# Performance work log

Hardware: AMD Instinct MI355X
Metric: run time of the kernel (lower is better)

The kernel has to match this reference:

```python
import jax, jax.numpy as jnp
import numpy as np

K = 20
SLOPE = 0.2  # LeakyReLU negative slope used by DGCNN edge convs


def _knn_idx(x, k):
    # x: [C, N]. Returns [N, k] indices of nearest neighbors by L2 distance
    # (includes self), matching torch topk of -pairwise_dist.
    xx = jnp.sum(x * x, axis=0)                      # [N]
    neg_dist = 2.0 * (x.T @ x) - xx[:, None] - xx[None, :]  # [N, N]
    return jax.lax.top_k(neg_dist, k)[1]


def _graph_feature(x, k):
    # x: [C, N] -> edge features [2C, N, k] = concat(x_j - x_i, x_i)
    idx = _knn_idx(x, k)                             # [N, k]
    nb = x[:, idx]                                   # [C, N, k] gather
    xc = jnp.broadcast_to(x[:, :, None], nb.shape)   # [C, N, k]
    return jnp.concatenate([nb - xc, xc], axis=0)


def _edge_conv(x, w, s, c, k):
    # 1x1 Conv2d (no bias) + eval-mode BN folded into per-channel (s, c)
    # + LeakyReLU, then max over the k neighbors.
    f = _graph_feature(x, k)                         # [2C, N, k]
    y = jnp.einsum('oc,cnk->onk', w, f)              # [Co, N, k]
    y = jax.nn.leaky_relu(y * s[:, None, None] + c[:, None, None], SLOPE)
    return jnp.max(y, axis=-1)                       # [Co, N]


def setup_inputs() -> dict:
    key = jax.random.key(0)
    ks = jax.random.split(key, 25)
    N = 16384
    f32 = jnp.float32

    def w(k, shape):
        return jax.random.normal(k, shape, dtype=f32) * 0.05

    def scale(k, shape):
        return 1.0 + 0.1 * jax.random.uniform(k, shape, dtype=f32)

    return {
        'coords': jax.random.normal(ks[0], (N, 3), dtype=f32),
        'feats': jax.random.uniform(ks[1], (N, 1), dtype=f32),
        'w1': w(ks[2], (64, 8)),    's1': scale(ks[3], (64,)),  'c1': w(ks[4], (64,)),
        'w2': w(ks[5], (64, 128)),  's2': scale(ks[6], (64,)),  'c2': w(ks[7], (64,)),
        'w3': w(ks[8], (128, 128)), 's3': scale(ks[9], (128,)), 'c3': w(ks[10], (128,)),
        'w4': w(ks[11], (256, 256)),'s4': scale(ks[12], (256,)),'c4': w(ks[13], (256,)),
        'w5': w(ks[14], (512, 512)),'s5': scale(ks[15], (512,)),'c5': w(ks[16], (512,)),
        'wf': w(ks[17], (3, 256, 512)), 'sf': scale(ks[18], (3, 256)), 'cf': w(ks[19], (3, 256)),
        'wsem': w(ks[20], (20, 256)), 'bsem': w(ks[21], (20,)),
    }


def reference(coords, feats, w1, s1, c1, w2, s2, c2, w3, s3, c3,
              w4, s4, c4, w5, s5, c5, wf, sf, cf, wsem, bsem):
    # Single-cloud batch (batch_size=1): x_input = cat(coords, feats).T -> [4, N]
    x0 = jnp.concatenate([coords.T, feats.T], axis=0)        # [4, N]
    x1 = _edge_conv(x0, w1, s1, c1, K)                       # [64, N]
    x2 = _edge_conv(x1, w2, s2, c2, K)                       # [64, N]
    x3 = _edge_conv(x2, w3, s3, c3, K)                       # [128, N]
    x4 = _edge_conv(x3, w4, s4, c4, K)                       # [256, N]
    cat = jnp.concatenate([x1, x2, x3, x4], axis=0)          # [512, N]
    x5 = jax.nn.leaky_relu(
        jnp.einsum('oc,cn->on', w5, cat) * s5[:, None] + c5[:, None], SLOPE)

    # Multi-scale feat_layers + out_bn (eval-mode BN folded to sf, cf)
    ms_feats = (jnp.einsum('soc,cn->son', wf, x5)
                * sf[:, :, None] + cf[:, :, None])           # [3, 256, N]

    # sem_head on the last scale's features
    sem_feat = ms_feats[-1].T                                # [N, 256]
    sem_logits = (sem_feat @ wsem.T + bsem)[None]            # [1, N, 20]

    ms_coords = jnp.broadcast_to(coords[None], (3,) + coords.shape)  # [3, N, 3]
    ms_masks = jnp.zeros((3, coords.shape[0]), dtype=bool)           # [3, N]
    return ms_feats, ms_coords, ms_masks, sem_logits
```

## Files before the change

kernel.cpp:

```cpp
#include <hip/hip_runtime.h>
#include <hip/hip_bf16.h>
#include <cmath>

#define K_NN 20
#define SLOPE 0.2f
#define NSEG 8
#define TK 16
#define SCAP 8

typedef _Float16 h8 __attribute__((ext_vector_type(8)));
typedef _Float16 h4 __attribute__((ext_vector_type(4)));
typedef float f4v __attribute__((ext_vector_type(4)));

__device__ __forceinline__ float lrelu(float x) { return x > 0.f ? x : SLOPE * x; }

__device__ __forceinline__ void topk_insert(float (&bd)[K_NN], int (&bi)[K_NN], float nd, int ji) {
  bool c[K_NN];
#pragma unroll
  for (int j = 0; j < K_NN; ++j) c[j] = nd > bd[j];
#pragma unroll
  for (int j = K_NN - 1; j >= 1; --j) {
    bd[j] = c[j] ? (c[j - 1] ? bd[j - 1] : nd) : bd[j];
    bi[j] = c[j] ? (c[j - 1] ? bi[j - 1] : ji) : bi[j];
  }
  bd[0] = c[0] ? nd : bd[0];
  bi[0] = c[0] ? ji : bi[0];
}

__global__ void build_x0_coords(const float* __restrict__ coords, const float* __restrict__ feats,
                                float* __restrict__ x0, float* __restrict__ oC,
                                float* __restrict__ oM, int N) {
  int n = blockIdx.x * 256 + threadIdx.x;
  if (n >= N) return;
  float c0 = coords[n * 3 + 0], c1 = coords[n * 3 + 1], c2 = coords[n * 3 + 2];
  float f = feats[n];
  float4 v = make_float4(c0, c1, c2, f);
  *(float4*)(x0 + (size_t)n * 4) = v;
#pragma unroll
  for (int s = 0; s < 3; ++s) {
    size_t b = (size_t)s * N * 3 + (size_t)n * 3;
    oC[b + 0] = c0; oC[b + 1] = c1; oC[b + 2] = c2;
    oM[(size_t)s * N + n] = 0.f;
  }
}

__global__ void compute_xx(const float* __restrict__ x, int ld, int C,
                           float* __restrict__ xx, int N) {
  int n = blockIdx.x * 256 + threadIdx.x;
  if (n >= N) return;
  const float* r = x + (size_t)n * ld;
  float s = 0.f;
  for (int c = 0; c < C; c += 4) {
    float4 v = *(const float4*)(r + c);
    s += v.x * v.x; s += v.y * v.y; s += v.z * v.z; s += v.w * v.w;
  }
  xx[n] = s;
}

template <int C>
__global__ void prep_hl(const float* __restrict__ x, int ld, _Float16* __restrict__ xh,
                        _Float16* __restrict__ xl, int N) {
  constexpr int C4 = C / 4;
  int i = blockIdx.x * 256 + threadIdx.x;
  if (i >= N * C4) return;
  int n = i / C4, c4 = i % C4;
  float4 v = *(const float4*)(x + (size_t)n * ld + c4 * 4);
  h4 hh, ll;
  hh[0] = (_Float16)v.x; ll[0] = (_Float16)(v.x - (float)hh[0]);
  hh[1] = (_Float16)v.y; ll[1] = (_Float16)(v.y - (float)hh[1]);
  hh[2] = (_Float16)v.z; ll[2] = (_Float16)(v.z - (float)hh[2]);
  hh[3] = (_Float16)v.w; ll[3] = (_Float16)(v.w - (float)hh[3]);
  *(h4*)(xh + (size_t)n * C + c4 * 4) = hh;
  *(h4*)(xl + (size_t)n * C + c4 * 4) = ll;
}

template <int C>
__global__ __launch_bounds__(256, 2) void knn_seg(
    const float* __restrict__ xP, int ld, const float* __restrict__ xx,
    float* __restrict__ pd, int* __restrict__ pi, int N, int segLen) {
  constexpr int T = 64;
  __shared__ float tile[T * C];
  __shared__ float txx[T];
  __shared__ float sd_st[SCAP * 256];
  __shared__ int si_st[SCAP * 256];
  int tid = threadIdx.x;
  int q = blockIdx.x * 256 + tid;
  int j0 = blockIdx.y * segLen;

  float4 qv[C / 4];
#pragma unroll
  for (int c4 = 0; c4 < C / 4; ++c4) qv[c4] = *(const float4*)(xP + (size_t)q * ld + c4 * 4);
  float xxq = xx[q];

  float bd[K_NN]; int bi[K_NN];
#pragma unroll
  for (int k = 0; k < K_NN; ++k) { bd[k] = -INFINITY; bi[k] = 0; }
  float thr = -INFINITY;
  int cnt = 0;

  for (int jt = j0; jt < j0 + segLen; jt += T) {
    constexpr int TOT4 = T * C / 4;
    for (int f = tid; f < TOT4; f += 256) {
      int t = f / (C / 4), c4 = f % (C / 4);
      *(float4*)(tile + t * C + c4 * 4) = *(const float4*)(xP + (size_t)(jt + t) * ld + c4 * 4);
    }
    if (tid < T) txx[tid] = xx[jt + tid];
    __syncthreads();
#pragma unroll 2
    for (int t = 0; t < T; ++t) {
      const float4* rp = (const float4*)(tile + t * C);
      float dot = 0.f;
#pragma unroll
      for (int c4 = 0; c4 < C / 4; ++c4) {
        float4 v = rp[c4];
        dot += qv[c4].x * v.x; dot += qv[c4].y * v.y;
        dot += qv[c4].z * v.z; dot += qv[c4].w * v.w;
      }
      float nd = 2.f * dot - xxq - txx[t];
      if (nd > thr) {
        sd_st[cnt * 256 + tid] = nd;
        si_st[cnt * 256 + tid] = jt + t;
        cnt++;
      }
      if (__any(cnt == SCAP)) {
        for (int e = 0; e < cnt; ++e) {
          float dnd = sd_st[e * 256 + tid];
          int dji = si_st[e * 256 + tid];
          if (dnd > bd[K_NN - 1]) topk_insert(bd, bi, dnd, dji);
        }
        cnt = 0;
        thr = bd[K_NN - 1];
      }
    }
    __syncthreads();
  }
  for (int e = 0; e < cnt; ++e) {
    float dnd = sd_st[e * 256 + tid];
    int dji = si_st[e * 256 + tid];
    if (dnd > bd[K_NN - 1]) topk_insert(bd, bi, dnd, dji);
  }

  size_t base = ((size_t)blockIdx.y * N + q) * K_NN;
#pragma unroll
  for (int k = 0; k < K_NN; ++k) { pd[base + k] = bd[k]; pi[base + k] = bi[k]; }
}

__global__ void knn_merge(const float* __restrict__ pd, const int* __restrict__ pi,
                          int* __restrict__ idx, int N, int S) {
  int q = blockIdx.x * 256 + threadIdx.x;
  if (q >= N) return;
  float bd[K_NN]; int bi[K_NN];
#pragma unroll
  for (int k = 0; k < K_NN; ++k) { bd[k] = -INFINITY; bi[k] = 0; }
  for (int s = 0; s < S; ++s) {
    size_t base = ((size_t)s * N + q) * K_NN;
    for (int k = 0; k < K_NN; ++k) {
      float nd = pd[base + k];
      if (!(nd > bd[K_NN - 1])) break;
      topk_insert(bd, bi, nd, pi[base + k]);
    }
  }
#pragma unroll
  for (int k = 0; k < K_NN; ++k) idx[(size_t)q * K_NN + k] = bi[k];
}

template <int C>
__global__ __launch_bounds__(512, 2) void knn_mfma(
    const _Float16* __restrict__ xh, const _Float16* __restrict__ xl,
    const float* __restrict__ xx, int* __restrict__ idx, int N) {
  constexpr int SLOTS = C / 8;
  constexpr int SWM = SLOTS - 1;
  constexpr int NCH = C / 32;
  constexpr int TILE_UNITS = 2 * 32 * SLOTS;
  constexpr int UPT = TILE_UNITS / 256;
  constexpr int STAGE_B = 2 * 2 * TILE_UNITS * 16;
  constexpr int MERGE_B = 64 * 8 * K_NN * 8;
  constexpr int LDS_B = (STAGE_B + 32768 > MERGE_B) ? STAGE_B + 32768 : MERGE_B;
  __shared__ char lds[LDS_B];
  float* sd_st = (float*)(lds + STAGE_B);
  int* si_st = (int*)(lds + STAGE_B + 16384);

  int tid = threadIdx.x;
  int wv = tid >> 6, lane = tid & 63;
  int qh = wv >> 1, ch = wv & 1;
  int lj = lane & 15, g = lane >> 4;
  int q0 = blockIdx.x * 64;
  int q = q0 + qh * 16 + lj;
  int chbase = ch * (N / 2);
  const int NT = (N / 2) / 32;

  h8 bh[NCH], bl[NCH];
#pragma unroll
  for (int m = 0; m < NCH; ++m) {
    bh[m] = *(const h8*)(xh + (size_t)q * C + m * 32 + g * 8);
    bl[m] = *(const h8*)(xl + (size_t)q * C + m * 32 + g * 8);
  }
  float qxx = xx[q];

  float bd[K_NN]; int bi[K_NN];
#pragma unroll
  for (int k = 0; k < K_NN; ++k) { bd[k] = -INFINITY; bi[k] = 0; }
  float thr = -INFINITY;
  int cnt = 0;

  int cidx = qh * 64 + lane;
  float4 ldr[UPT];

  auto ldreg = [&](int t) {
    int jt = chbase + t * 32;
#pragma unroll
    for (int u = 0; u < UPT; ++u) {
      int p = cidx * UPT + u;
      int part = p / (32 * SLOTS);
      int row = (p / SLOTS) & 31;
      int slot = p & SWM;
      const _Float16* src = part ? xl : xh;
      ldr[u] = *(const float4*)(src + (size_t)(jt + row) * C + (slot ^ (row & SWM)) * 8);
    }
  };
  auto dswrite = [&](int buf) {
#pragma unroll
    for (int u = 0; u < UPT; ++u) {
      int p = cidx * UPT + u;
      *(float4*)(lds + ((size_t)(ch * 2 + buf) * TILE_UNITS + p) * 16) = ldr[u];
    }
  };
  auto compute = [&](int buf, int jt) {
    float cxx[8];
#pragma unroll
    for (int s = 0; s < 2; ++s)
#pragma unroll
      for (int r = 0; r < 4; ++r) cxx[s * 4 + r] = xx[jt + s * 16 + g * 4 + r];
    char* tb = lds + (size_t)(ch * 2 + buf) * TILE_UNITS * 16;
#pragma unroll
    for (int sub = 0; sub < 2; ++sub) {
      int row = sub * 16 + lj;
      h8 ah[NCH], al[NCH];
#pragma unroll
      for (int m = 0; m < NCH; ++m) {
        int su = (m * 4 + g) ^ (row & SWM);
        ah[m] = *(const h8*)(tb + ((size_t)(0 * 32 + row) * SLOTS + su) * 16);
        al[m] = *(const h8*)(tb + ((size_t)(1 * 32 + row) * SLOTS + su) * 16);
      }
      f4v acc = {0.f, 0.f, 0.f, 0.f};
#pragma unroll
      for (int m = 0; m < NCH; ++m)
        acc = __builtin_amdgcn_mfma_f32_16x16x32_f16(ah[m], bh[m], acc, 0, 0, 0);
#pragma unroll
      for (int m = 0; m < NCH; ++m)
        acc = __builtin_amdgcn_mfma_f32_16x16x32_f16(ah[m], bl[m], acc, 0, 0, 0);
#pragma unroll
      for (int m = 0; m < NCH; ++m)
        acc = __builtin_amdgcn_mfma_f32_16x16x32_f16(al[m], bh[m], acc, 0, 0, 0);
#pragma unroll
      for (int r = 0; r < 4; ++r) {
        float d = 2.f * acc[r] - qxx - cxx[sub * 4 + r];
        if (d > thr) {
          sd_st[cnt * 512 + tid] = d;
          si_st[cnt * 512 + tid] = jt + sub * 16 + g * 4 + r;
          cnt++;
        }
        if (__any(cnt == SCAP)) {
          for (int e = 0; e < cnt; ++e) {
            float dnd = sd_st[e * 512 + tid];
            int dji = si_st[e * 512 + tid];
            if (dnd > bd[K_NN - 1]) topk_insert(bd, bi, dnd, dji);
          }
          cnt = 0;
          thr = bd[K_NN - 1];
        }
      }
    }
  };

  ldreg(0);
  dswrite(0);
  __syncthreads();
  for (int t = 0; t < NT; ++t) {
    int cur = t & 1;
    if (t + 1 < NT) ldreg(t + 1);
    compute(cur, chbase + t * 32);
    __syncthreads();
    if (t + 1 < NT) {
      dswrite(cur ^ 1);
      __syncthreads();
    }
  }
  for (int e = 0; e < cnt; ++e) {
    float dnd = sd_st[e * 512 + tid];
    int dji = si_st[e * 512 + tid];
    if (dnd > bd[K_NN - 1]) topk_insert(bd, bi, dnd, dji);
  }
  __syncthreads();

  float* mg = (float*)lds;
  int list = ch * 4 + g;
  int qlocal = qh * 16 + lj;
#pragma unroll
  for (int k = 0; k < K_NN; ++k) {
    int e = ((qlocal * 8 + list) * K_NN + k) * 2;
    mg[e] = bd[k];
    ((int*)mg)[e + 1] = bi[k];
  }
  __syncthreads();
  if (tid < 64) {
    int pr[8] = {0, 0, 0, 0, 0, 0, 0, 0};
    float hd[8]; int hx[8];
#pragma unroll
    for (int j = 0; j < 8; ++j) {
      int e = ((tid * 8 + j) * K_NN) * 2;
      hd[j] = mg[e]; hx[j] = ((int*)mg)[e + 1];
    }
    for (int k = 0; k < K_NN; ++k) {
      float best = hd[0]; int bidx = hx[0]; int bj = 0;
#pragma unroll
      for (int j = 1; j < 8; ++j) {
        bool btr = (hd[j] > best) || (hd[j] == best && hx[j] < bidx);
        best = btr ? hd[j] : best;
        bidx = btr ? hx[j] : bidx;
        bj = btr ? j : bj;
      }
      idx[(size_t)(q0 + tid) * K_NN + k] = bidx;
#pragma unroll
      for (int j = 0; j < 8; ++j) {
        if (j == bj) {
          pr[j]++;
          if (pr[j] < K_NN) {
            int e = ((tid * 8 + j) * K_NN + pr[j]) * 2;
            hd[j] = mg[e]; hx[j] = ((int*)mg)[e + 1];
          } else {
            hd[j] = -INFINITY; hx[j] = 0x7fffffff;
          }
        }
      }
    }
  }
}

__global__ void prep_wcat(const float* __restrict__ w, float* __restrict__ wcat, int O, int C) {
  int i = blockIdx.x * 256 + threadIdx.x;
  if (i >= O * C) return;
  int o = i / C, c = i % C;
  float wa = w[(size_t)o * 2 * C + c];
  float wb = w[(size_t)o * 2 * C + C + c];
  wcat[(size_t)o * C + c] = wa;
  wcat[((size_t)O + o) * C + c] = wb - wa;
}

template <int MODE>
__global__ __launch_bounds__(256) void gemm_nt(
    const float* __restrict__ A, int lda, const float* __restrict__ B, int ldb,
    float* __restrict__ Out, int ldo, int M, int Nout, int Kdim,
    const float* __restrict__ sv, const float* __restrict__ cv) {
  __shared__ float As[TK][64];
  __shared__ float Bs[TK][64];
  int tid = threadIdx.x;
  int tx = tid & 15, ty = tid >> 4;
  int m0 = blockIdx.x * 64, n0 = blockIdx.y * 64;
  int lrow = tid >> 2, lkq = tid & 3;
  float acc[4][4] = {};

  for (int k0 = 0; k0 < Kdim; k0 += TK) {
    float4 av = make_float4(0.f, 0.f, 0.f, 0.f), bv = make_float4(0.f, 0.f, 0.f, 0.f);
    if (k0 + lkq * 4 < Kdim) {
      av = *(const float4*)(A + (size_t)(m0 + lrow) * lda + k0 + lkq * 4);
      bv = *(const float4*)(B + (size_t)(n0 + lrow) * ldb + k0 + lkq * 4);
    }
    As[lkq * 4 + 0][lrow] = av.x; As[lkq * 4 + 1][lrow] = av.y;
    As[lkq * 4 + 2][lrow] = av.z; As[lkq * 4 + 3][lrow] = av.w;
    Bs[lkq * 4 + 0][lrow] = bv.x; Bs[lkq * 4 + 1][lrow] = bv.y;
    Bs[lkq * 4 + 2][lrow] = bv.z; Bs[lkq * 4 + 3][lrow] = bv.w;
    __syncthreads();
#pragma unroll
    for (int kk = 0; kk < TK; ++kk) {
      float a[4], b[4];
      *(float4*)a = *(const float4*)&As[kk][ty * 4];
      *(float4*)b = *(const float4*)&Bs[kk][tx * 4];
#pragma unroll
      for (int i = 0; i < 4; ++i)
#pragma unroll
        for (int j = 0; j < 4; ++j) acc[i][j] += a[i] * b[j];
    }
    __syncthreads();
  }

  float4 s4 = make_float4(1.f, 1.f, 1.f, 1.f), c4 = make_float4(0.f, 0.f, 0.f, 0.f);
  if (MODE != 0) {
    s4 = *(const float4*)(sv + n0 + tx * 4);
    c4 = *(const float4*)(cv + n0 + tx * 4);
  }
#pragma unroll
  for (int i = 0; i < 4; ++i) {
    float4 r = make_float4(acc[i][0], acc[i][1], acc[i][2], acc[i][3]);
    if (MODE != 0) {
      r.x = r.x * s4.x + c4.x; r.y = r.y * s4.y + c4.y;
      r.z = r.z * s4.z + c4.z; r.w = r.w * s4.w + c4.w;
    }
    if (MODE == 1) { r.x = lrelu(r.x); r.y = lrelu(r.y); r.z = lrelu(r.z); r.w = lrelu(r.w); }
    *(float4*)(Out + (size_t)(m0 + ty * 4 + i) * ldo + n0 + tx * 4) = r;
  }
}

template <int O>
__global__ void edge_max(const float* __restrict__ U, const int* __restrict__ idx,
                         const float* __restrict__ sv, const float* __restrict__ cv,
                         float* __restrict__ out, int N) {
  constexpr int TPP = O / 4;
  constexpr int PPB = 256 / TPP;
  int tid = threadIdx.x;
  int n = blockIdx.x * PPB + tid / TPP;
  int o4 = tid % TPP;
  const int* ir = idx + (size_t)n * K_NN;
  float4 m = make_float4(-INFINITY, -INFINITY, -INFINITY, -INFINITY);
#pragma unroll
  for (int k = 0; k < K_NN; ++k) {
    int j = ir[k];
    float4 t = *(const float4*)(U + (size_t)j * (2 * O) + o4 * 4);
    m.x = fmaxf(m.x, t.x); m.y = fmaxf(m.y, t.y);
    m.z = fmaxf(m.z, t.z); m.w = fmaxf(m.w, t.w);
  }
  float4 v = *(const float4*)(U + (size_t)n * (2 * O) + O + o4 * 4);
  float4 s4 = *(const float4*)(sv + o4 * 4);
  float4 c4 = *(const float4*)(cv + o4 * 4);
  float4 r;
  r.x = lrelu(s4.x * (v.x + m.x) + c4.x);
  r.y = lrelu(s4.y * (v.y + m.y) + c4.y);
  r.z = lrelu(s4.z * (v.z + m.z) + c4.z);
  r.w = lrelu(s4.w * (v.w + m.w) + c4.w);
  *(float4*)(out + (size_t)n * 512 + o4 * 4) = r;
}

__global__ void transpose_nt(const float* __restrict__ in, float* __restrict__ out, int N, int Cc) {
  __shared__ float t[32][33];
  int bx = blockIdx.x, by = blockIdx.y;
  int lx = threadIdx.x, ly = threadIdx.y;
#pragma unroll
  for (int i = 0; i < 4; ++i)
    t[ly + i * 8][lx] = in[(size_t)(by * 32 + ly + i * 8) * Cc + bx * 32 + lx];
  __syncthreads();
#pragma unroll
  for (int i = 0; i < 4; ++i)
    out[(size_t)(bx * 32 + ly + i * 8) * N + by * 32 + lx] = t[lx][ly + i * 8];
}

__global__ void sem_kernel(const float* __restrict__ T1, const float* __restrict__ wsem,
                           const float* __restrict__ bsem, float* __restrict__ out, int N) {
  int tid = threadIdx.x;
  int n = blockIdx.x * 8 + (tid >> 5);
  int g = tid & 31;
  if (g < 20) {
    const float* row = T1 + (size_t)n * 768 + 512;
    const float* wr = wsem + (size_t)g * 256;
    float acc = 0.f;
    for (int o = 0; o < 256; ++o) acc += row[o] * wr[o];
    out[(size_t)n * 20 + g] = acc + bsem[g];
  }
}

template <int C, int O>
static void run_layer_seg(const float* x, int ld, const float* wc, const float* sv,
                          const float* cv, float* outcol, float* xxb, int* idxb, float* pd,
                          int* pi, float* U, int N, hipStream_t stream) {
  compute_xx<<<N / 256, 256, 0, stream>>>(x, ld, C, xxb, N);
  knn_seg<C><<<dim3(N / 256, NSEG), 256, 0, stream>>>(x, ld, xxb, pd, pi, N, N / NSEG);
  knn_merge<<<N / 256, 256, 0, stream>>>(pd, pi, idxb, N, NSEG);
  gemm_nt<0><<<dim3(N / 64, (2 * O) / 64), 256, 0, stream>>>(x, ld, wc, C, U, 2 * O, N, 2 * O, C,
                                                             nullptr, nullptr);
  edge_max<O><<<N / (256 / (O / 4)), 256, 0, stream>>>(U, idxb, sv, cv, outcol, N);
}

template <int C, int O>
static void run_layer_mfma(const float* x, int ld, const float* wc, const float* sv,
                           const float* cv, float* outcol, float* xxb, int* idxb,
                           _Float16* xh, _Float16* xl, float* U, int N, hipStream_t stream) {
  compute_xx<<<N / 256, 256, 0, stream>>>(x, ld, C, xxb, N);
  prep_hl<C><<<(N * (C / 4)) / 256, 256, 0, stream>>>(x, ld, xh, xl, N);
  knn_mfma<C><<<N / 64, 512, 0, stream>>>(xh, xl, xxb, idxb, N);
  gemm_nt<0><<<dim3(N / 64, (2 * O) / 64), 256, 0, stream>>>(x, ld, wc, C, U, 2 * O, N, 2 * O, C,
                                                             nullptr, nullptr);
  edge_max<O><<<N / (256 / (O / 4)), 256, 0, stream>>>(U, idxb, sv, cv, outcol, N);
}

extern "C" void kernel_launch(void* const* d_in, const int* in_sizes, int n_in,
                              void* d_out, int out_size, void* d_ws, size_t ws_size,
                              hipStream_t stream) {
  const int N = in_sizes[0] / 3;
  const float* coords = (const float*)d_in[0];
  const float* feats  = (const float*)d_in[1];
  const float* w1 = (const float*)d_in[2];
  const float* s1 = (const float*)d_in[3];
  const float* c1 = (const float*)d_in[4];
  const float* w2 = (const float*)d_in[5];
  const float* s2 = (const float*)d_in[6];
  const float* c2 = (const float*)d_in[7];
  const float* w3 = (const float*)d_in[8];
  const float* s3 = (const float*)d_in[9];
  const float* c3 = (const float*)d_in[10];
  const float* w4 = (const float*)d_in[11];
  const float* s4 = (const float*)d_in[12];
  const float* c4 = (const float*)d_in[13];
  const float* w5 = (const float*)d_in[14];
  const float* s5 = (const float*)d_in[15];
  const float* c5 = (const float*)d_in[16];
  const float* wf = (const float*)d_in[17];
  const float* sf = (const float*)d_in[18];
  const float* cf = (const float*)d_in[19];
  const float* wsem = (const float*)d_in[20];
  const float* bsem = (const float*)d_in[21];

  float* base = (float*)d_ws;
  size_t off = 0;
  float* XC  = base + off; off += (size_t)N * 512;
  float* UX5 = base + off; off += (size_t)N * 512;
  float* x0  = base + off; off += (size_t)N * 4;
  float* xxb = base + off; off += (size_t)N;
  int*   idxb = (int*)(base + off); off += (size_t)N * K_NN;
  float* wc1 = base + off; off += 128 * 4;
  float* wc2 = base + off; off += 128 * 64;
  float* wc3 = base + off; off += 256 * 64;
  float* wc4 = base + off; off += 512 * 128;
  float* T1  = base + off; off += (size_t)N * 768;
  float* pd = T1;
  int*   pi = (int*)(T1 + (size_t)NSEG * N * K_NN);
  _Float16* xh = (_Float16*)UX5;
  _Float16* xl = (_Float16*)(UX5 + (size_t)N * 64);

  float* oF = (float*)d_out;
  float* oC = oF + (size_t)3 * 256 * N;
  float* oM = oC + (size_t)3 * N * 3;
  float* oL = oM + (size_t)3 * N;

  build_x0_coords<<<N / 256, 256, 0, stream>>>(coords, feats, x0, oC, oM, N);

  prep_wcat<<<(64 * 4 + 255) / 256, 256, 0, stream>>>(w1, wc1, 64, 4);
  prep_wcat<<<(64 * 64 + 255) / 256, 256, 0, stream>>>(w2, wc2, 64, 64);
  prep_wcat<<<(128 * 64 + 255) / 256, 256, 0, stream>>>(w3, wc3, 128, 64);
  prep_wcat<<<(256 * 128 + 255) / 256, 256, 0, stream>>>(w4, wc4, 256, 128);

  run_layer_seg<4, 64>(x0, 4, wc1, s1, c1, XC + 0, xxb, idxb, pd, pi, UX5, N, stream);
  run_layer_mfma<64, 64>(XC + 0, 512, wc2, s2, c2, XC + 64, xxb, idxb, xh, xl, UX5, N, stream);
  run_layer_mfma<64, 128>(XC + 64, 512, wc3, s3, c3, XC + 128, xxb, idxb, xh, xl, UX5, N, stream);
  run_layer_mfma<128, 256>(XC + 128, 512, wc4, s4, c4, XC + 256, xxb, idxb, xh, xl, UX5, N, stream);

  gemm_nt<1><<<dim3(N / 64, 8), 256, 0, stream>>>(XC, 512, w5, 512, UX5, 512, N, 512, 512, s5, c5);
  gemm_nt<2><<<dim3(N / 64, 12), 256, 0, stream>>>(UX5, 512, wf, 512, T1, 768, N, 768, 512, sf, cf);
  transpose_nt<<<dim3(24, N / 32), dim3(32, 8), 0, stream>>>(T1, oF, N, 768);
  sem_kernel<<<N / 8, 256, 0, stream>>>(T1, wsem, bsem, oL, N);
}
```

Baseline: 4.065 ms.

## Shrink knn_mfma LDS footprint and move partial-list merge to separate kernel

The in-kernel 8-way merge of partial top-k lists, which needed a large LDS region, is removed. Each wave now writes its sorted partial list to global scratch, and the existing knn_merge kernel combines them afterward. The candidate staging buffer is cut from 8 to 4 entries per thread, which flushes more often, and the tile load mapping changes to a coalesced u*256+cidx pattern. Together these lower LDS use so more blocks can be resident, at the cost of extra global traffic and another kernel launch.

Result: slower. 4.262 ms (+4.8%).

```diff
diff --git a/kernel.cpp b/kernel.cpp
--- a/kernel.cpp
+++ b/kernel.cpp
@@ -7,6 +7,7 @@
 #define NSEG 8
 #define TK 16
 #define SCAP 8
+#define SCAP_M 4
 
 typedef _Float16 h8 __attribute__((ext_vector_type(8)));
 typedef _Float16 h4 __attribute__((ext_vector_type(4)));
@@ -167,18 +168,16 @@
 template <int C>
 __global__ __launch_bounds__(512, 2) void knn_mfma(
     const _Float16* __restrict__ xh, const _Float16* __restrict__ xl,
-    const float* __restrict__ xx, int* __restrict__ idx, int N) {
+    const float* __restrict__ xx, float* __restrict__ pd, int* __restrict__ pi, int N) {
   constexpr int SLOTS = C / 8;
   constexpr int SWM = SLOTS - 1;
   constexpr int NCH = C / 32;
   constexpr int TILE_UNITS = 2 * 32 * SLOTS;
   constexpr int UPT = TILE_UNITS / 256;
   constexpr int STAGE_B = 2 * 2 * TILE_UNITS * 16;
-  constexpr int MERGE_B = 64 * 8 * K_NN * 8;
-  constexpr int LDS_B = (STAGE_B + 32768 > MERGE_B) ? STAGE_B + 32768 : MERGE_B;
-  __shared__ char lds[LDS_B];
-  float* sd_st = (float*)(lds + STAGE_B);
-  int* si_st = (int*)(lds + STAGE_B + 16384);
+  __shared__ char lds[STAGE_B];
+  __shared__ float sd_st[SCAP_M * 512];
+  __shared__ int si_st[SCAP_M * 512];
 
   int tid = threadIdx.x;
   int wv = tid >> 6, lane = tid & 63;
@@ -210,7 +209,7 @@
     int jt = chbase + t * 32;
 #pragma unroll
     for (int u = 0; u < UPT; ++u) {
-      int p = cidx * UPT + u;
+      int p = u * 256 + cidx;
       int part = p / (32 * SLOTS);
       int row = (p / SLOTS) & 31;
       int slot = p & SWM;
@@ -221,7 +220,7 @@
   auto dswrite = [&](int buf) {
 #pragma unroll
     for (int u = 0; u < UPT; ++u) {
-      int p = cidx * UPT + u;
+      int p = u * 256 + cidx;
       *(float4*)(lds + ((size_t)(ch * 2 + buf) * TILE_UNITS + p) * 16) = ldr[u];
     }
   };
@@ -260,7 +259,7 @@
           si_st[cnt * 512 + tid] = jt + sub * 16 + g * 4 + r;
           cnt++;
         }
-        if (__any(cnt == SCAP)) {
+        if (__any(cnt == SCAP_M)) {
           for (int e = 0; e < cnt; ++e) {
             float dnd = sd_st[e * 512 + tid];
             int dji = si_st[e * 512 + tid];
@@ -291,50 +290,11 @@
     int dji = si_st[e * 512 + tid];
     if (dnd > bd[K_NN - 1]) topk_insert(bd, bi, dnd, dji);
   }
-  __syncthreads();
-
-  float* mg = (float*)lds;
+
   int list = ch * 4 + g;
-  int qlocal = qh * 16 + lj;
-#pragma unroll
-  for (int k = 0; k < K_NN; ++k) {
-    int e = ((qlocal * 8 + list) * K_NN + k) * 2;
-    mg[e] = bd[k];
-    ((int*)mg)[e + 1] = bi[k];
-  }
-  __syncthreads();
-  if (tid < 64) {
-    int pr[8] = {0, 0, 0, 0, 0, 0, 0, 0};
-    float hd[8]; int hx[8];
-#pragma unroll
-    for (int j = 0; j < 8; ++j) {
-      int e = ((tid * 8 + j) * K_NN) * 2;
-      hd[j] = mg[e]; hx[j] = ((int*)mg)[e + 1];
-    }
-    for (int k = 0; k < K_NN; ++k) {
-      float best = hd[0]; int bidx = hx[0]; int bj = 0;
-#pragma unroll
-      for (int j = 1; j < 8; ++j) {
-        bool btr = (hd[j] > best) || (hd[j] == best && hx[j] < bidx);
-        best = btr ? hd[j] : best;
-        bidx = btr ? hx[j] : bidx;
-        bj = btr ? j : bj;
-      }
-      idx[(size_t)(q0 + tid) * K_NN + k] = bidx;
-#pragma unroll
-      for (int j = 0; j < 8; ++j) {
-        if (j == bj) {
-          pr[j]++;
-          if (pr[j] < K_NN) {
-            int e = ((tid * 8 + j) * K_NN + pr[j]) * 2;
-            hd[j] = mg[e]; hx[j] = ((int*)mg)[e + 1];
-          } else {
-            hd[j] = -INFINITY; hx[j] = 0x7fffffff;
-          }
-        }
-      }
-    }
-  }
+  size_t base = ((size_t)list * N + q) * K_NN;
+#pragma unroll
+  for (int k = 0; k < K_NN; ++k) { pd[base + k] = bd[k]; pi[base + k] = bi[k]; }
 }
 
 __global__ void prep_wcat(const float* __restrict__ w, float* __restrict__ wcat, int O, int C) {
@@ -471,11 +431,13 @@
 
 template <int C, int O>
 static void run_layer_mfma(const float* x, int ld, const float* wc, const float* sv,
-                           const float* cv, float* outcol, float* xxb, int* idxb,
-                           _Float16* xh, _Float16* xl, float* U, int N, hipStream_t stream) {
+                           const float* cv, float* outcol, float* xxb, int* idxb, float* pd,
+                           int* pi, _Float16* xh, _Float16* xl, float* U, int N,
+                           hipStream_t stream) {
   compute_xx<<<N / 256, 256, 0, stream>>>(x, ld, C, xxb, N);
   prep_hl<C><<<(N * (C / 4)) / 256, 256, 0, stream>>>(x, ld, xh, xl, N);
-  knn_mfma<C><<<N / 64, 512, 0, stream>>>(xh, xl, xxb, idxb, N);
+  knn_mfma<C><<<N / 64, 512, 0, stream>>>(xh, xl, xxb, pd, pi, N);
+  knn_merge<<<N / 256, 256, 0, stream>>>(pd, pi, idxb, N, 8);
   gemm_nt<0><<<dim3(N / 64, (2 * O) / 64), 256, 0, stream>>>(x, ld, wc, C, U, 2 * O, N, 2 * O, C,
                                                              nullptr, nullptr);
   edge_max<O><<<N / (256 / (O / 4)), 256, 0, stream>>>(U, idxb, sv, cv, outcol, N);
@@ -538,9 +500,9 @@
   prep_wcat<<<(256 * 128 + 255) / 256, 256, 0, stream>>>(w4, wc4, 256, 128);
 
   run_layer_seg<4, 64>(x0, 4, wc1, s1, c1, XC + 0, xxb, idxb, pd, pi, UX5, N, stream);
-  run_layer_mfma<64, 64>(XC + 0, 512, wc2, s2, c2, XC + 64, xxb, idxb, xh, xl, UX5, N, stream);
-  run_layer_mfma<64, 128>(XC + 64, 512, wc3, s3, c3, XC + 128, xxb, idxb, xh, xl, UX5, N, stream);
-  run_layer_mfma<128, 256>(XC + 128, 512, wc4, s4, c4, XC + 256, xxb, idxb, xh, xl, UX5, N, stream);
+  run_layer_mfma<64, 64>(XC + 0, 512, wc2, s2, c2, XC + 64, xxb, idxb, pd, pi, xh, xl, UX5, N, stream);
+  run_layer_mfma<64, 128>(XC + 64, 512, wc3, s3, c3, XC + 128, xxb, idxb, pd, pi, xh, xl, UX5, N, stream);
+  run_layer_mfma<128, 256>(XC + 128, 512, wc4, s4, c4, XC + 256, xxb, idxb, pd, pi, xh, xl, UX5, N, stream);
 
   gemm_nt<1><<<dim3(N / 64, 8), 256, 0, stream>>>(XC, 512, w5, 512, UX5, 512, N, 512, 512, s5, c5);
   gemm_nt<2><<<dim3(N / 64, 12), 256, 0, stream>>>(UX5, 512, wf, 512, T1, 768, N, 768, 512, sf, cf);
```
